# Performance work log

Hardware: AMD Instinct MI355X
Metric: run time of the kernel (lower is better)

Reference implementation:

```python
import jax, jax.numpy as jnp
import numpy as np

N = 50000        # nodes
E = 800000       # edges (avg degree 16)
D_IN = 19        # in_channels(16) + 2 coords + 1 observed flag
H = 64           # graph_hidden
L = 3            # graph_layers
EPS = 1e-5       # BatchNorm eps


def setup_inputs() -> dict:
    key = jax.random.key(0)
    ks = jax.random.split(key, 12)
    s = 0.05
    x = jax.random.normal(ks[0], (N, D_IN), jnp.float32)
    edge_index = jax.random.randint(ks[1], (2, E), 0, N, dtype=jnp.int32)
    return {
        "x": x,
        "edge_index": edge_index,
        # input projection + input BN
        "w_in": jax.random.normal(ks[2], (D_IN, H), jnp.float32) * s,
        "b_in": jnp.zeros((H,), jnp.float32),
        "bn0_g": jnp.ones((H,), jnp.float32),
        "bn0_b": jnp.zeros((H,), jnp.float32),
        # per-layer SAGEConv: lin_l (aggregated neighbors, with bias), lin_r (self, no bias)
        "wl": jax.random.normal(ks[3], (L, H, H), jnp.float32) * s,
        "bl": jnp.zeros((L, H), jnp.float32),
        "wr": jax.random.normal(ks[4], (L, H, H), jnp.float32) * s,
        # per-layer BatchNorm affine
        "bn_g": jnp.ones((L, H), jnp.float32),
        "bn_b": jnp.zeros((L, H), jnp.float32),
    }


def _batchnorm(h, g, b):
    # training-mode BN over the node axis (biased variance, like torch)
    mu = h.mean(axis=0)
    var = h.var(axis=0)
    return (h - mu) * jax.lax.rsqrt(var + EPS) * g + b


def reference(x, edge_index, w_in, b_in, bn0_g, bn0_b, wl, bl, wr, bn_g, bn_b):
    src = edge_index[0]
    dst = edge_index[1]
    n = x.shape[0]

    # input_proj -> BN -> ReLU  (dropout is identity at inference)
    h = x @ w_in + b_in
    h = jax.nn.relu(_batchnorm(h, bn0_g, bn0_b))

    # in-degree for mean aggregation (computed once)
    deg = jax.ops.segment_sum(jnp.ones((src.shape[0],), h.dtype), dst, num_segments=n)
    denom = jnp.maximum(deg, 1.0)[:, None]

    for l in range(L):
        # SAGEConv(mean): gather source feats, segment-mean into targets
        msgs = h[src]                                        # [E, H] gather
        agg = jax.ops.segment_sum(msgs, dst, num_segments=n) / denom
        h_new = agg @ wl[l] + bl[l] + h @ wr[l]
        h_new = jax.nn.relu(_batchnorm(h_new, bn_g[l], bn_b[l]))
        h = h + h_new                                        # residual
    return h
```

## Files before the change

kernel.cpp:

```cpp
#include <hip/hip_runtime.h>
#include <hip/hip_bf16.h>

#define NODES 50000
#define EDGES 800000
#define DIN   19
#define LAYERS 3
#define BN_EPS 1e-5f

#define NBINS 196
#define EPB   4096
#define NBLK  196
#define NTILES 782
#define G0TILES 196
#define APPLY_BLOCKS 2048
#define TPB   256

typedef __attribute__((ext_vector_type(4))) float f32x4;
typedef __attribute__((ext_vector_type(2))) float f32x2;
typedef __attribute__((ext_vector_type(8))) short s16x8;

__device__ inline ushort bf16bits(float f) {
    __hip_bfloat16 h = __float2bfloat16(f);
    return *reinterpret_cast<ushort*>(&h);
}

#if __has_builtin(__builtin_amdgcn_cvt_pk_f32_fp8) && __has_builtin(__builtin_amdgcn_cvt_pk_fp8_f32)
__device__ inline unsigned pack4_fp8(float a, float b, float c, float d) {
    unsigned w = __builtin_amdgcn_cvt_pk_fp8_f32(a, b, 0u, false);
    return __builtin_amdgcn_cvt_pk_fp8_f32(c, d, w, true);
}
__device__ inline void acc4_fp8(unsigned v, float& a0, float& a1, float& a2, float& a3) {
    f32x2 lo = __builtin_amdgcn_cvt_pk_f32_fp8(v, false);
    f32x2 hi = __builtin_amdgcn_cvt_pk_f32_fp8(v, true);
    a0 += lo.x; a1 += lo.y; a2 += hi.x; a3 += hi.y;
}
#else
__device__ inline unsigned enc1(float f) {
    _Float16 hf = (_Float16)f;
    unsigned u = (unsigned)*reinterpret_cast<unsigned short*>(&hf);
    u = (u + 0x7Fu + ((u >> 8) & 1u)) >> 8;
    return u & 0xFFu;
}
__device__ inline float dec1(unsigned b) {
    unsigned short u = (unsigned short)(b << 8);
    _Float16 hf = *reinterpret_cast<_Float16*>(&u);
    return (float)hf;
}
__device__ inline unsigned pack4_fp8(float a, float b, float c, float d) {
    return enc1(a) | (enc1(b) << 8) | (enc1(c) << 16) | (enc1(d) << 24);
}
__device__ inline void acc4_fp8(unsigned v, float& a0, float& a1, float& a2, float& a3) {
    a0 += dec1(v & 0xFF); a1 += dec1((v >> 8) & 0xFF);
    a2 += dec1((v >> 16) & 0xFF); a3 += dec1(v >> 24);
}
#endif


__global__ void k_prep(const float* __restrict__ w_in, const float* __restrict__ wl,
                       const float* __restrict__ wr, ushort* __restrict__ WiT,
                       ushort* __restrict__ WcatT, int* __restrict__ bintot,
                       float* __restrict__ stats) {
    int i0 = blockIdx.x * blockDim.x + threadIdx.x;
    int stride = gridDim.x * blockDim.x;
    for (int i = i0; i < NBINS; i += stride) bintot[i] = 0;
    for (int i = i0; i < 4 * 2048; i += stride) stats[i] = 0.0f;
    for (int i = i0; i < 64 * 32; i += stride) {
        int c = i >> 5, k = i & 31;
        WiT[i] = bf16bits(k < DIN ? w_in[k * 64 + c] : 0.0f);
    }
    for (int i = i0; i < LAYERS * 64 * 128; i += stride) {
        int l = i >> 13, rem = i & 8191;
        int c = rem >> 7, k = rem & 127;
        float v = (k < 64) ? wl[(l * 64 + k) * 64 + c] : wr[(l * 64 + (k - 64)) * 64 + c];
        WcatT[i] = bf16bits(v);
    }
}


union SMemK2 {
    struct { int hist[256], cur[256], wsum[4]; unsigned stage[EPB]; } sort;
    struct { ushort xt[256][40]; float red[4][4][128]; } g0;
};

__device__ inline void do_sortA(int blk, int t, const int* __restrict__ src,
                                const int* __restrict__ dst, int2* __restrict__ cb,
                                int* __restrict__ bintot, unsigned* __restrict__ bbuf,
                                SMemK2& sm) {
    int e0 = blk * EPB;
    int ne = min(EPB, EDGES - e0);
    int d[4]; unsigned pk[4];
    #pragma unroll
    for (int i = 0; i < 4; ++i) {
        int j = t + i * 1024;
        if (j < ne) {
            int dd = dst[e0 + j];
            d[i] = dd;
            pk[i] = ((unsigned)(dd & 255) << 24) | (unsigned)src[e0 + j];
        } else d[i] = -1;
    }
    if (t < 256) sm.sort.hist[t] = 0;
    __syncthreads();
    #pragma unroll
    for (int i = 0; i < 4; ++i)
        if (d[i] >= 0) atomicAdd(&sm.sort.hist[d[i] >> 8], 1);
    __syncthreads();
    int ln = t & 63, wv = t >> 6;
    int cntv = 0, inc = 0;
    if (t < 256) {
        cntv = sm.sort.hist[t];
        inc = cntv;
        #pragma unroll
        for (int s = 1; s < 64; s <<= 1) {
            int u = __shfl_up(inc, s);
            if (ln >= s) inc += u;
        }
        if (ln == 63) sm.sort.wsum[wv] = inc;
    }
    __syncthreads();
    if (t < 256) {
        int woff = 0;
        #pragma unroll
        for (int i = 0; i < 4; ++i) if (i < wv) woff += sm.sort.wsum[i];
        int excl = woff + inc - cntv;
        sm.sort.cur[t] = excl;
        if (t < NBINS) {
            cb[t * NBLK + blk] = make_int2(excl, cntv);
            if (cntv) atomicAdd(&bintot[t], cntv);
        }
    }
    __syncthreads();
    #pragma unroll
    for (int i = 0; i < 4; ++i)
        if (d[i] >= 0) {
            int slot = atomicAdd(&sm.sort.cur[d[i] >> 8], 1);
            sm.sort.stage[slot] = pk[i];
        }
    __syncthreads();
    #pragma unroll
    for (int i = 0; i < 4; ++i) {
        int j = t + i * 1024;
        if (j < ne) bbuf[e0 + j] = sm.sort.stage[j];
    }
}

__device__ inline void do_gemm0(int tile, int t, const float* __restrict__ x,
                                const ushort* __restrict__ WiT, const float* __restrict__ bias,
                                ushort* __restrict__ tb, float* __restrict__ stats,
                                SMemK2& sm) {
    int base = tile * 256;
    int nv = min(256, NODES - base);
    unsigned* xz = (unsigned*)sm.g0.xt;
    for (int i = t; i < 256 * 20; i += 1024) xz[i] = 0;
    __syncthreads();
    const float* xs = x + (size_t)base * DIN;
    for (int e = t; e < nv * DIN; e += 1024) {
        int n = e / DIN, k = e - n * DIN;
        sm.g0.xt[n][k] = bf16bits(xs[e]);
    }
    __syncthreads();
    int grp = t >> 8, tl = t & 255;
    int lane = t & 63, wl = (tl >> 6);
    int r = lane & 15, g = lane >> 4;
    f32x4 acc[4] = {{0.f,0.f,0.f,0.f},{0.f,0.f,0.f,0.f},{0.f,0.f,0.f,0.f},{0.f,0.f,0.f,0.f}};
    s16x8 af = *(const s16x8*)&sm.g0.xt[grp * 64 + wl * 16 + r][g * 8];
    #pragma unroll
    for (int j = 0; j < 4; ++j) {
        s16x8 bf = *(const s16x8*)(WiT + (size_t)(j * 16 + r) * 32 + g * 8);
        acc[j] = __builtin_amdgcn_mfma_f32_16x16x32_bf16(af, bf, acc[j], 0, 0, 0);
    }
    int row0 = base + grp * 64 + wl * 16;
    float s_[4], q_[4];
    #pragma unroll
    for (int j = 0; j < 4; ++j) {
        float b = bias[j * 16 + r];
        float s = 0.0f, q = 0.0f;
        #pragma unroll
        for (int i = 0; i < 4; ++i) {
            int row = row0 + g * 4 + i;
            if (row < NODES) {
                float v = acc[j][i] + b;
                tb[(size_t)row * 64 + j * 16 + r] = bf16bits(v);
                s += v; q += v * v;
            }
        }
        s += __shfl_xor(s, 16); s += __shfl_xor(s, 32);
        q += __shfl_xor(q, 16); q += __shfl_xor(q, 32);
        s_[j] = s; q_[j] = q;
    }
    if (g == 0) {
        #pragma unroll
        for (int j = 0; j < 4; ++j) {
            sm.g0.red[grp][wl][j * 16 + r] = s_[j];
            sm.g0.red[grp][wl][64 + j * 16 + r] = q_[j];
        }
    }
    __syncthreads();
    if (tl < 128) {
        float tot = sm.g0.red[grp][0][tl] + sm.g0.red[grp][1][tl] +
                    sm.g0.red[grp][2][tl] + sm.g0.red[grp][3][tl];
        atomicAdd(&stats[tl * 16], tot);
    }
}

__global__ __launch_bounds__(1024) void k_sort_g0(const int* __restrict__ esrc, const int* __restrict__ edst,
                                                  int2* __restrict__ cb, int* __restrict__ bintot,
                                                  unsigned* __restrict__ bbuf,
                                                  const float* __restrict__ x, const ushort* __restrict__ WiT,
                                                  const float* __restrict__ bias, ushort* __restrict__ tb,
                                                  float* __restrict__ stats) {
    __shared__ SMemK2 sm;
    int t = threadIdx.x;
    if (blockIdx.x < NBLK) do_sortA(blockIdx.x, t, esrc, edst, cb, bintot, bbuf, sm);
    else                   do_gemm0(blockIdx.x - NBLK, t, x, WiT, bias, tb, stats, sm);
}


__device__ inline int ubound(const int* pre, int f) {
    int lo = 0, hi = NBLK;
    while (lo + 1 < hi) {
        int mid = (lo + hi) >> 1;
        if (pre[mid] <= f) lo = mid; else hi = mid;
    }
    return lo;
}

struct SMemBinB {
    int red[256];
    int segoff[NBLK], segcnt[NBLK], pre[NBLK + 1];
    int deg[256], loff[256], cur[256];
    int wsum4[4];
};

__device__ inline void do_binB(int b, int t, const int2* __restrict__ cb,
                               const int* __restrict__ bintot, const unsigned* __restrict__ bbuf,
                               int* __restrict__ off, float* __restrict__ rden,
                               int* __restrict__ ebuf, SMemBinB& sm) {
    int ln = t & 63, wv = t >> 6;
    sm.red[t] = (t < b) ? bintot[t] : 0;
    __syncthreads();
    #pragma unroll
    for (int s = 128; s > 0; s >>= 1) {
        if (t < s) sm.red[t] += sm.red[t + s];
        __syncthreads();
    }
    int binoff = sm.red[0];
    if (t < NBLK) {
        int2 c = cb[b * NBLK + t];
        sm.segoff[t] = c.x; sm.segcnt[t] = c.y;
    }
    sm.deg[t] = 0; sm.cur[t] = 0;
    __syncthreads();
    if (wv == 0) {
        int carry = 0;
        for (int base = 0; base < NBLK; base += 64) {
            int idx = base + ln;
            int v = (idx < NBLK) ? sm.segcnt[idx] : 0;
            int inc = v;
            #pragma unroll
            for (int s = 1; s < 64; s <<= 1) {
                int u = __shfl_up(inc, s);
                if (ln >= s) inc += u;
            }
            if (idx < NBLK) sm.pre[idx] = carry + inc - v;
            carry += __shfl(inc, 63);
        }
        if (ln == 0) sm.pre[NBLK] = carry;
    }
    __syncthreads();
    int total = sm.pre[NBLK];
    for (int f = t; f < total; f += TPB) {
        int sg = ubound(sm.pre, f);
        unsigned e = bbuf[sg * EPB + sm.segoff[sg] + (f - sm.pre[sg])];
        atomicAdd(&sm.deg[e >> 24], 1);
    }
    __syncthreads();
    int dv = sm.deg[t], inc2 = dv;
    #pragma unroll
    for (int s = 1; s < 64; s <<= 1) {
        int u = __shfl_up(inc2, s);
        if (ln >= s) inc2 += u;
    }
    if (ln == 63) sm.wsum4[wv] = inc2;
    __syncthreads();
    int woff = 0;
    #pragma unroll
    for (int i = 0; i < 4; ++i) if (i < wv) woff += sm.wsum4[i];
    int excl = woff + inc2 - dv;
    sm.loff[t] = excl;
    int node = (b << 8) + t;
    if (node < NODES) {
        off[node] = binoff + excl;
        rden[node] = 1.0f / fmaxf((float)dv, 1.0f);
    }
    if (b == NBINS - 1 && t == 0) off[NODES] = EDGES;
    __syncthreads();
    for (int f = t; f < total; f += TPB) {
        int sg = ubound(sm.pre, f);
        unsigned e = bbuf[sg * EPB + sm.segoff[sg] + (f - sm.pre[sg])];
        int dd = e >> 24;
        int slot = atomicAdd(&sm.cur[dd], 1);
        ebuf[binoff + sm.loff[dd] + slot] = (int)(e & 0xFFFFFFu);
    }
}

__device__ inline void do_apply(int idx0, int stride, const ushort* __restrict__ tb,
                                const float* __restrict__ stats, const float* __restrict__ gamma,
                                const float* __restrict__ beta, float* __restrict__ h,
                                ushort* __restrict__ AB, unsigned* __restrict__ hb8,
                                int residual, int write_next) {
    const float invN = 1.0f / NODES;
    for (int idx = idx0; idx < NODES * 16; idx += stride) {
        int n = idx >> 4;
        int j = (idx & 15) * 4;
        ushort4 tv = *(const ushort4*)(tb + (size_t)n * 64 + j);
        float tf[4] = { __uint_as_float((unsigned)tv.x << 16), __uint_as_float((unsigned)tv.y << 16),
                        __uint_as_float((unsigned)tv.z << 16), __uint_as_float((unsigned)tv.w << 16) };
        f32x4 hv;
        if (residual) hv = *(const f32x4*)(h + (size_t)n * 64 + j);
        float out[4];
        ushort ub[4];
        #pragma unroll
        for (int k = 0; k < 4; ++k) {
            int f = j + k;
            float mu = stats[f * 16] * invN;
            float var = stats[(64 + f) * 16] * invN - mu * mu;
            float sc = gamma[f] * rsqrtf(var + BN_EPS);
            float sh = beta[f] - mu * sc;
            float v = fmaxf(tf[k] * sc + sh, 0.0f);
            out[k] = residual ? (hv[k] + v) : v;
            ub[k] = bf16bits(out[k]);
        }
        *(f32x4*)(h + (size_t)n * 64 + j) = f32x4{out[0], out[1], out[2], out[3]};
        if (write_next) {
            *(ushort4*)(AB + (size_t)n * 128 + 64 + j) = make_ushort4(ub[0], ub[1], ub[2], ub[3]);
            hb8[(size_t)n * 16 + (idx & 15)] = pack4_fp8(out[0], out[1], out[2], out[3]);
        }
    }
}

__global__ __launch_bounds__(TPB) void k_csr_bn0(const int2* __restrict__ cb, const int* __restrict__ bintot,
                                                 const unsigned* __restrict__ bbuf,
                                                 int* __restrict__ off, float* __restrict__ rden,
                                                 int* __restrict__ ebuf,
                                                 const ushort* __restrict__ tb, const float* __restrict__ stats,
                                                 const float* __restrict__ gamma, const float* __restrict__ beta,
                                                 float* __restrict__ h, ushort* __restrict__ AB,
                                                 unsigned* __restrict__ hb8) {
    __shared__ SMemBinB sm;
    int t = threadIdx.x;
    if (blockIdx.x < NBINS) {
        do_binB(blockIdx.x, t, cb, bintot, bbuf, off, rden, ebuf, sm);
    } else {
        int vb = blockIdx.x - NBINS;
        do_apply(vb * TPB + t, APPLY_BLOCKS * TPB, tb, stats, gamma, beta, h, AB, hb8, 0, 1);
    }
}


__global__ __launch_bounds__(TPB) void k_gemm(const ushort* __restrict__ AB, const ushort* __restrict__ WT,
                                              const float* __restrict__ bias, ushort* __restrict__ tb,
                                              float* __restrict__ stats) {
    __shared__ float red[4][128];
    int t = threadIdx.x;
    int lane = t & 63, wave = t >> 6;
    int row0 = blockIdx.x * 64;
    int r = lane & 15, g = lane >> 4;
    f32x4 acc[4] = {{0.f,0.f,0.f,0.f},{0.f,0.f,0.f,0.f},{0.f,0.f,0.f,0.f},{0.f,0.f,0.f,0.f}};
    int ar = row0 + wave * 16 + r;
    if (ar >= NODES) ar = NODES - 1;
    #pragma unroll
    for (int k0 = 0; k0 < 128; k0 += 32) {
        s16x8 af = *(const s16x8*)(AB + (size_t)ar * 128 + k0 + g * 8);
        #pragma unroll
        for (int j = 0; j < 4; ++j) {
            s16x8 bf = *(const s16x8*)(WT + (size_t)(j * 16 + r) * 128 + k0 + g * 8);
            acc[j] = __builtin_amdgcn_mfma_f32_16x16x32_bf16(af, bf, acc[j], 0, 0, 0);
        }
    }
    float s_[4], q_[4];
    #pragma unroll
    for (int j = 0; j < 4; ++j) {
        float b = bias[j * 16 + r];
        float s = 0.0f, q = 0.0f;
        #pragma unroll
        for (int i = 0; i < 4; ++i) {
            int row = row0 + wave * 16 + g * 4 + i;
            if (row < NODES) {
                float v = acc[j][i] + b;
                tb[(size_t)row * 64 + j * 16 + r] = bf16bits(v);
                s += v; q += v * v;
            }
        }
        s += __shfl_xor(s, 16); s += __shfl_xor(s, 32);
        q += __shfl_xor(q, 16); q += __shfl_xor(q, 32);
        s_[j] = s; q_[j] = q;
    }
    if (g == 0) {
        #pragma unroll
        for (int j = 0; j < 4; ++j) {
            red[wave][j * 16 + r] = s_[j];
            red[wave][64 + j * 16 + r] = q_[j];
        }
    }
    __syncthreads();
    if (t < 128) {
        float tot = red[0][t] + red[1][t] + red[2][t] + red[3][t];
        atomicAdd(&stats[t * 16], tot);
    }
}


__global__ void k_apply(const ushort* __restrict__ tb, const float* __restrict__ stats,
                        const float* __restrict__ gamma, const float* __restrict__ beta,
                        float* __restrict__ h, ushort* __restrict__ AB,
                        unsigned* __restrict__ hb8, int residual, int write_next) {
    do_apply(blockIdx.x * blockDim.x + threadIdx.x, gridDim.x * blockDim.x,
             tb, stats, gamma, beta, h, AB, hb8, residual, write_next);
}


__global__ void k_agg(const int* __restrict__ off, const int* __restrict__ ebuf,
                      const float* __restrict__ rden, const unsigned* __restrict__ hb8,
                      ushort* __restrict__ ABh) {
    unsigned* AB = (unsigned*)ABh;
    int t = threadIdx.x;
    int lane = t & 63;
    int q = lane >> 4;
    int fl = lane & 15;
    int w = blockIdx.x * (blockDim.x >> 6) + (t >> 6);
    int nw = gridDim.x * (blockDim.x >> 6);
    for (int n = w; n < NODES; n += nw) {
        int p0 = off[n], p1 = off[n + 1];
        float a0 = 0.f, a1 = 0.f, a2 = 0.f, a3 = 0.f;
        int p = p0 + q;
        for (; p + 12 < p1; p += 16) {
            int s0 = ebuf[p], s1 = ebuf[p + 4], s2 = ebuf[p + 8], s3 = ebuf[p + 12];
            unsigned v0 = hb8[(size_t)s0 * 16 + fl];
            unsigned v1 = hb8[(size_t)s1 * 16 + fl];
            unsigned v2 = hb8[(size_t)s2 * 16 + fl];
            unsigned v3 = hb8[(size_t)s3 * 16 + fl];
            acc4_fp8(v0, a0, a1, a2, a3);
            acc4_fp8(v1, a0, a1, a2, a3);
            acc4_fp8(v2, a0, a1, a2, a3);
            acc4_fp8(v3, a0, a1, a2, a3);
        }
        for (; p < p1; p += 4) {
            unsigned v = hb8[(size_t)ebuf[p] * 16 + fl];
            acc4_fp8(v, a0, a1, a2, a3);
        }
        a0 += __shfl_xor(a0, 16); a0 += __shfl_xor(a0, 32);
        a1 += __shfl_xor(a1, 16); a1 += __shfl_xor(a1, 32);
        a2 += __shfl_xor(a2, 16); a2 += __shfl_xor(a2, 32);
        a3 += __shfl_xor(a3, 16); a3 += __shfl_xor(a3, 32);
        if (q == 0) {
            float rd = rden[n];
            uint2 o;
            o.x = (unsigned)bf16bits(a0 * rd) | ((unsigned)bf16bits(a1 * rd) << 16);
            o.y = (unsigned)bf16bits(a2 * rd) | ((unsigned)bf16bits(a3 * rd) << 16);
            *(uint2*)(AB + (size_t)n * 64 + fl * 2) = o;
        }
    }
}


extern "C" void kernel_launch(void* const* d_in, const int* in_sizes, int n_in,
                              void* d_out, int out_size, void* d_ws, size_t ws_size,
                              hipStream_t stream) {
    const float* x    = (const float*)d_in[0];
    const int*   ei   = (const int*)d_in[1];
    const float* w_in = (const float*)d_in[2];
    const float* b_in = (const float*)d_in[3];
    const float* bn0g = (const float*)d_in[4];
    const float* bn0b = (const float*)d_in[5];
    const float* wl   = (const float*)d_in[6];
    const float* bl   = (const float*)d_in[7];
    const float* wr   = (const float*)d_in[8];
    const float* bng  = (const float*)d_in[9];
    const float* bnb  = (const float*)d_in[10];
    const int* esrc = ei;
    const int* edst = ei + EDGES;
    float* h = (float*)d_out;

    char* p = (char*)d_ws;
    auto alloc = [&](size_t bytes) {
        char* r = p;
        p += (bytes + 255) & ~size_t(255);
        return r;
    };
    int*      bintot = (int*)alloc((size_t)NBINS * 4);
    float*    stats  = (float*)alloc((size_t)4 * 2048 * 4);
    int2*     cb     = (int2*)alloc((size_t)NBINS * NBLK * 8);
    unsigned* bbuf   = (unsigned*)alloc((size_t)NBLK * EPB * 4);
    int*      off    = (int*)alloc((size_t)(NODES + 1) * 4);
    float*    rden   = (float*)alloc((size_t)NODES * 4);
    int*      ebuf   = (int*)alloc((size_t)EDGES * 4);
    ushort*   WiT    = (ushort*)alloc(64 * 32 * 2);
    ushort*   WcatT  = (ushort*)alloc(LAYERS * 64 * 128 * 2);
    ushort*   tb     = (ushort*)alloc((size_t)NODES * 64 * 2);
    ushort*   AB     = (ushort*)alloc((size_t)NODES * 128 * 2);
    unsigned* hb8    = (unsigned*)alloc((size_t)NODES * 16 * 4);

    k_prep<<<128, TPB, 0, stream>>>(w_in, wl, wr, WiT, WcatT, bintot, stats);
    k_sort_g0<<<NBLK + G0TILES, 1024, 0, stream>>>(esrc, edst, cb, bintot, bbuf,
                                                   x, WiT, b_in, tb, stats);
    k_csr_bn0<<<NBINS + APPLY_BLOCKS, TPB, 0, stream>>>(cb, bintot, bbuf, off, rden, ebuf,
                                                        tb, stats, bn0g, bn0b, h, AB, hb8);

    for (int l = 0; l < LAYERS; ++l) {
        k_agg<<<2048, TPB, 0, stream>>>(off, ebuf, rden, hb8, AB);
        k_gemm<<<NTILES, TPB, 0, stream>>>(AB, WcatT + l * 8192, bl + l * 64,
                                           tb, stats + (l + 1) * 2048);
        k_apply<<<APPLY_BLOCKS, TPB, 0, stream>>>(tb, stats + (l + 1) * 2048, bng + l * 64,
                                                  bnb + l * 64, h, AB, hb8, 1,
                                                  l < LAYERS - 1 ? 1 : 0);
    }
}
```

Measured before the change: 279.1 us.

## Fuse self-term GEMM into BN apply and widen aggregation gathers

The BN/ReLU/residual apply pass now also computes the next layer's self term (h @ wr + bias) with MFMA on a 64-row tile held in shared memory, storing it as a bf16 buffer. The layer GEMM then only multiplies the 64-wide aggregated features and adds that precomputed term, so the bf16 copy of h in the concatenated AB buffer is no longer written or re-read. The aggregation kernel is restructured so each lane gathers 8 fp8 bytes per edge, with 8 edges in flight per wave. The cost is an extra bf16 intermediate rounding of the self term, plus fewer apply blocks (one per 64-row tile instead of a grid-stride loop).

```diff
diff --git a/kernel.cpp b/kernel.cpp
--- a/kernel.cpp
+++ b/kernel.cpp
@@ -12,7 +12,6 @@
 #define NBLK  196
 #define NTILES 782
 #define G0TILES 196
-#define APPLY_BLOCKS 2048
 #define TPB   256
 
 typedef __attribute__((ext_vector_type(4))) float f32x4;
@@ -23,16 +22,17 @@
     __hip_bfloat16 h = __float2bfloat16(f);
     return *reinterpret_cast<ushort*>(&h);
 }
+__device__ inline float bf16val(ushort u) { return __uint_as_float((unsigned)u << 16); }
 
 #if __has_builtin(__builtin_amdgcn_cvt_pk_f32_fp8) && __has_builtin(__builtin_amdgcn_cvt_pk_fp8_f32)
 __device__ inline unsigned pack4_fp8(float a, float b, float c, float d) {
     unsigned w = __builtin_amdgcn_cvt_pk_fp8_f32(a, b, 0u, false);
     return __builtin_amdgcn_cvt_pk_fp8_f32(c, d, w, true);
 }
-__device__ inline void acc4_fp8(unsigned v, float& a0, float& a1, float& a2, float& a3) {
+__device__ inline void acc4_fp8(unsigned v, float* a) {
     f32x2 lo = __builtin_amdgcn_cvt_pk_f32_fp8(v, false);
     f32x2 hi = __builtin_amdgcn_cvt_pk_f32_fp8(v, true);
-    a0 += lo.x; a1 += lo.y; a2 += hi.x; a3 += hi.y;
+    a[0] += lo.x; a[1] += lo.y; a[2] += hi.x; a[3] += hi.y;
 }
 #else
 __device__ inline unsigned enc1(float f) {
@@ -49,9 +49,9 @@
 __device__ inline unsigned pack4_fp8(float a, float b, float c, float d) {
     return enc1(a) | (enc1(b) << 8) | (enc1(c) << 16) | (enc1(d) << 24);
 }
-__device__ inline void acc4_fp8(unsigned v, float& a0, float& a1, float& a2, float& a3) {
-    a0 += dec1(v & 0xFF); a1 += dec1((v >> 8) & 0xFF);
-    a2 += dec1((v >> 16) & 0xFF); a3 += dec1(v >> 24);
+__device__ inline void acc4_fp8(unsigned v, float* a) {
+    a[0] += dec1(v & 0xFF); a[1] += dec1((v >> 8) & 0xFF);
+    a[2] += dec1((v >> 16) & 0xFF); a[3] += dec1(v >> 24);
 }
 #endif
 
@@ -215,6 +215,75 @@
 }
 
 
+struct SMemApplyR {
+    ushort hn[64][72];
+};
+
+__device__ inline void do_applyR(int rb, int t, int l,
+                                 const ushort* __restrict__ tb, const float* __restrict__ stats,
+                                 const float* __restrict__ gamma, const float* __restrict__ beta,
+                                 float* __restrict__ h, unsigned* __restrict__ hb8,
+                                 const ushort* __restrict__ WcatT, const float* __restrict__ bl,
+                                 ushort* __restrict__ tb2, int residual, SMemApplyR& sm) {
+    const float invN = 1.0f / NODES;
+    int base = rb * 64;
+    int nv = min(64, NODES - base);
+    for (int idx = t; idx < nv * 16; idx += TPB) {
+        int n = base + (idx >> 4);
+        int j = (idx & 15) * 4;
+        ushort4 tv = *(const ushort4*)(tb + (size_t)n * 64 + j);
+        float tf[4] = { bf16val(tv.x), bf16val(tv.y), bf16val(tv.z), bf16val(tv.w) };
+        f32x4 hv;
+        if (residual) hv = *(const f32x4*)(h + (size_t)n * 64 + j);
+        float out[4];
+        #pragma unroll
+        for (int k = 0; k < 4; ++k) {
+            int f = j + k;
+            float mu = stats[f * 16] * invN;
+            float var = stats[(64 + f) * 16] * invN - mu * mu;
+            float sc = gamma[f] * rsqrtf(var + BN_EPS);
+            float sh = beta[f] - mu * sc;
+            float v = fmaxf(tf[k] * sc + sh, 0.0f);
+            out[k] = residual ? (hv[k] + v) : v;
+            sm.hn[idx >> 4][j + k] = bf16bits(out[k]);
+        }
+        *(f32x4*)(h + (size_t)n * 64 + j) = f32x4{out[0], out[1], out[2], out[3]};
+        hb8[(size_t)n * 16 + (idx & 15)] = pack4_fp8(out[0], out[1], out[2], out[3]);
+    }
+    __syncthreads();
+    int lane = t & 63, wave = t >> 6;
+    int r = lane & 15, g = lane >> 4;
+    f32x4 acc[4] = {{0.f,0.f,0.f,0.f},{0.f,0.f,0.f,0.f},{0.f,0.f,0.f,0.f},{0.f,0.f,0.f,0.f}};
+    #pragma unroll
+    for (int k0 = 0; k0 < 64; k0 += 32) {
+        s16x8 af = *(const s16x8*)&sm.hn[wave * 16 + r][k0 + g * 8];
+        #pragma unroll
+        for (int j = 0; j < 4; ++j) {
+            s16x8 bf = *(const s16x8*)(WcatT + (size_t)l * 8192 + (size_t)(j * 16 + r) * 128 + 64 + k0 + g * 8);
+            acc[j] = __builtin_amdgcn_mfma_f32_16x16x32_bf16(af, bf, acc[j], 0, 0, 0);
+        }
+    }
+    #pragma unroll
+    for (int j = 0; j < 4; ++j) {
+        float b = bl[j * 16 + r];
+        #pragma unroll
+        for (int i = 0; i < 4; ++i) {
+            int row = base + wave * 16 + g * 4 + i;
+            if (row < NODES) tb2[(size_t)row * 64 + j * 16 + r] = bf16bits(acc[j][i] + b);
+        }
+    }
+}
+
+__global__ __launch_bounds__(TPB) void k_applyR(const ushort* __restrict__ tb, const float* __restrict__ stats,
+                                                const float* __restrict__ gamma, const float* __restrict__ beta,
+                                                float* __restrict__ h, unsigned* __restrict__ hb8,
+                                                const ushort* __restrict__ WcatT, const float* __restrict__ bl,
+                                                ushort* __restrict__ tb2, int l, int residual) {
+    __shared__ SMemApplyR sm;
+    do_applyR(blockIdx.x, threadIdx.x, l, tb, stats, gamma, beta, h, hb8, WcatT, bl, tb2, residual, sm);
+}
+
+
 __device__ inline int ubound(const int* pre, int f) {
     int lo = 0, hi = NBLK;
     while (lo + 1 < hi) {
@@ -229,6 +298,11 @@
     int segoff[NBLK], segcnt[NBLK], pre[NBLK + 1];
     int deg[256], loff[256], cur[256];
     int wsum4[4];
+};
+
+union SMemK3 {
+    SMemBinB binb;
+    SMemApplyR ar;
 };
 
 __device__ inline void do_binB(int b, int t, const int2* __restrict__ cb,
@@ -303,63 +377,27 @@
     }
 }
 
-__device__ inline void do_apply(int idx0, int stride, const ushort* __restrict__ tb,
-                                const float* __restrict__ stats, const float* __restrict__ gamma,
-                                const float* __restrict__ beta, float* __restrict__ h,
-                                ushort* __restrict__ AB, unsigned* __restrict__ hb8,
-                                int residual, int write_next) {
-    const float invN = 1.0f / NODES;
-    for (int idx = idx0; idx < NODES * 16; idx += stride) {
-        int n = idx >> 4;
-        int j = (idx & 15) * 4;
-        ushort4 tv = *(const ushort4*)(tb + (size_t)n * 64 + j);
-        float tf[4] = { __uint_as_float((unsigned)tv.x << 16), __uint_as_float((unsigned)tv.y << 16),
-                        __uint_as_float((unsigned)tv.z << 16), __uint_as_float((unsigned)tv.w << 16) };
-        f32x4 hv;
-        if (residual) hv = *(const f32x4*)(h + (size_t)n * 64 + j);
-        float out[4];
-        ushort ub[4];
-        #pragma unroll
-        for (int k = 0; k < 4; ++k) {
-            int f = j + k;
-            float mu = stats[f * 16] * invN;
-            float var = stats[(64 + f) * 16] * invN - mu * mu;
-            float sc = gamma[f] * rsqrtf(var + BN_EPS);
-            float sh = beta[f] - mu * sc;
-            float v = fmaxf(tf[k] * sc + sh, 0.0f);
-            out[k] = residual ? (hv[k] + v) : v;
-            ub[k] = bf16bits(out[k]);
-        }
-        *(f32x4*)(h + (size_t)n * 64 + j) = f32x4{out[0], out[1], out[2], out[3]};
-        if (write_next) {
-            *(ushort4*)(AB + (size_t)n * 128 + 64 + j) = make_ushort4(ub[0], ub[1], ub[2], ub[3]);
-            hb8[(size_t)n * 16 + (idx & 15)] = pack4_fp8(out[0], out[1], out[2], out[3]);
-        }
-    }
-}
-
-__global__ __launch_bounds__(TPB) void k_csr_bn0(const int2* __restrict__ cb, const int* __restrict__ bintot,
+__global__ __launch_bounds__(TPB) void k_csr_ar0(const int2* __restrict__ cb, const int* __restrict__ bintot,
                                                  const unsigned* __restrict__ bbuf,
                                                  int* __restrict__ off, float* __restrict__ rden,
                                                  int* __restrict__ ebuf,
                                                  const ushort* __restrict__ tb, const float* __restrict__ stats,
                                                  const float* __restrict__ gamma, const float* __restrict__ beta,
-                                                 float* __restrict__ h, ushort* __restrict__ AB,
-                                                 unsigned* __restrict__ hb8) {
-    __shared__ SMemBinB sm;
+                                                 float* __restrict__ h, unsigned* __restrict__ hb8,
+                                                 const ushort* __restrict__ WcatT, const float* __restrict__ bl,
+                                                 ushort* __restrict__ tb2) {
+    __shared__ SMemK3 sm;
     int t = threadIdx.x;
-    if (blockIdx.x < NBINS) {
-        do_binB(blockIdx.x, t, cb, bintot, bbuf, off, rden, ebuf, sm);
-    } else {
-        int vb = blockIdx.x - NBINS;
-        do_apply(vb * TPB + t, APPLY_BLOCKS * TPB, tb, stats, gamma, beta, h, AB, hb8, 0, 1);
-    }
-}
-
-
-__global__ __launch_bounds__(TPB) void k_gemm(const ushort* __restrict__ AB, const ushort* __restrict__ WT,
-                                              const float* __restrict__ bias, ushort* __restrict__ tb,
-                                              float* __restrict__ stats) {
+    if (blockIdx.x < NBINS)
+        do_binB(blockIdx.x, t, cb, bintot, bbuf, off, rden, ebuf, sm.binb);
+    else
+        do_applyR(blockIdx.x - NBINS, t, 0, tb, stats, gamma, beta, h, hb8, WcatT, bl, tb2, 0, sm.ar);
+}
+
+
+__global__ __launch_bounds__(TPB) void k_gemmL(const ushort* __restrict__ AB, const ushort* __restrict__ WcatT,
+                                               const ushort* __restrict__ tb2, ushort* __restrict__ tb,
+                                               float* __restrict__ stats, int l) {
     __shared__ float red[4][128];
     int t = threadIdx.x;
     int lane = t & 63, wave = t >> 6;
@@ -369,24 +407,23 @@
     int ar = row0 + wave * 16 + r;
     if (ar >= NODES) ar = NODES - 1;
     #pragma unroll
-    for (int k0 = 0; k0 < 128; k0 += 32) {
-        s16x8 af = *(const s16x8*)(AB + (size_t)ar * 128 + k0 + g * 8);
+    for (int k0 = 0; k0 < 64; k0 += 32) {
+        s16x8 af = *(const s16x8*)(AB + (size_t)ar * 64 + k0 + g * 8);
         #pragma unroll
         for (int j = 0; j < 4; ++j) {
-            s16x8 bf = *(const s16x8*)(WT + (size_t)(j * 16 + r) * 128 + k0 + g * 8);
+            s16x8 bf = *(const s16x8*)(WcatT + (size_t)l * 8192 + (size_t)(j * 16 + r) * 128 + k0 + g * 8);
             acc[j] = __builtin_amdgcn_mfma_f32_16x16x32_bf16(af, bf, acc[j], 0, 0, 0);
         }
     }
     float s_[4], q_[4];
     #pragma unroll
     for (int j = 0; j < 4; ++j) {
-        float b = bias[j * 16 + r];
         float s = 0.0f, q = 0.0f;
         #pragma unroll
         for (int i = 0; i < 4; ++i) {
             int row = row0 + wave * 16 + g * 4 + i;
             if (row < NODES) {
-                float v = acc[j][i] + b;
+                float v = acc[j][i] + bf16val(tb2[(size_t)row * 64 + j * 16 + r]);
                 tb[(size_t)row * 64 + j * 16 + r] = bf16bits(v);
                 s += v; q += v * v;
             }
@@ -410,54 +447,73 @@
 }
 
 
-__global__ void k_apply(const ushort* __restrict__ tb, const float* __restrict__ stats,
-                        const float* __restrict__ gamma, const float* __restrict__ beta,
-                        float* __restrict__ h, ushort* __restrict__ AB,
-                        unsigned* __restrict__ hb8, int residual, int write_next) {
-    do_apply(blockIdx.x * blockDim.x + threadIdx.x, gridDim.x * blockDim.x,
-             tb, stats, gamma, beta, h, AB, hb8, residual, write_next);
+__global__ void k_apply_fin(const ushort* __restrict__ tb, const float* __restrict__ stats,
+                            const float* __restrict__ gamma, const float* __restrict__ beta,
+                            float* __restrict__ h) {
+    int idx0 = blockIdx.x * blockDim.x + threadIdx.x;
+    int stride = gridDim.x * blockDim.x;
+    const float invN = 1.0f / NODES;
+    for (int idx = idx0; idx < NODES * 16; idx += stride) {
+        int n = idx >> 4;
+        int j = (idx & 15) * 4;
+        ushort4 tv = *(const ushort4*)(tb + (size_t)n * 64 + j);
+        float tf[4] = { bf16val(tv.x), bf16val(tv.y), bf16val(tv.z), bf16val(tv.w) };
+        f32x4 hv = *(const f32x4*)(h + (size_t)n * 64 + j);
+        float out[4];
+        #pragma unroll
+        for (int k = 0; k < 4; ++k) {
+            int f = j + k;
+            float mu = stats[f * 16] * invN;
+            float var = stats[(64 + f) * 16] * invN - mu * mu;
+            float sc = gamma[f] * rsqrtf(var + BN_EPS);
+            float sh = beta[f] - mu * sc;
+            out[k] = hv[k] + fmaxf(tf[k] * sc + sh, 0.0f);
+        }
+        *(f32x4*)(h + (size_t)n * 64 + j) = f32x4{out[0], out[1], out[2], out[3]};
+    }
 }
 
 
 __global__ void k_agg(const int* __restrict__ off, const int* __restrict__ ebuf,
                       const float* __restrict__ rden, const unsigned* __restrict__ hb8,
                       ushort* __restrict__ ABh) {
-    unsigned* AB = (unsigned*)ABh;
+    const uint2* H2 = (const uint2*)hb8;
+    uint4* AB4 = (uint4*)ABh;
     int t = threadIdx.x;
     int lane = t & 63;
-    int q = lane >> 4;
-    int fl = lane & 15;
+    int q = lane >> 3;
+    int fl = lane & 7;
     int w = blockIdx.x * (blockDim.x >> 6) + (t >> 6);
     int nw = gridDim.x * (blockDim.x >> 6);
     for (int n = w; n < NODES; n += nw) {
         int p0 = off[n], p1 = off[n + 1];
-        float a0 = 0.f, a1 = 0.f, a2 = 0.f, a3 = 0.f;
+        float a[8] = {0.f,0.f,0.f,0.f,0.f,0.f,0.f,0.f};
         int p = p0 + q;
-        for (; p + 12 < p1; p += 16) {
-            int s0 = ebuf[p], s1 = ebuf[p + 4], s2 = ebuf[p + 8], s3 = ebuf[p + 12];
-            unsigned v0 = hb8[(size_t)s0 * 16 + fl];
-            unsigned v1 = hb8[(size_t)s1 * 16 + fl];
-            unsigned v2 = hb8[(size_t)s2 * 16 + fl];
-            unsigned v3 = hb8[(size_t)s3 * 16 + fl];
-            acc4_fp8(v0, a0, a1, a2, a3);
-            acc4_fp8(v1, a0, a1, a2, a3);
-            acc4_fp8(v2, a0, a1, a2, a3);
-            acc4_fp8(v3, a0, a1, a2, a3);
-        }
-        for (; p < p1; p += 4) {
-            unsigned v = hb8[(size_t)ebuf[p] * 16 + fl];
-            acc4_fp8(v, a0, a1, a2, a3);
-        }
-        a0 += __shfl_xor(a0, 16); a0 += __shfl_xor(a0, 32);
-        a1 += __shfl_xor(a1, 16); a1 += __shfl_xor(a1, 32);
-        a2 += __shfl_xor(a2, 16); a2 += __shfl_xor(a2, 32);
-        a3 += __shfl_xor(a3, 16); a3 += __shfl_xor(a3, 32);
+        for (; p + 8 < p1; p += 16) {
+            int s0 = ebuf[p], s1 = ebuf[p + 8];
+            uint2 v0 = H2[(size_t)s0 * 8 + fl];
+            uint2 v1 = H2[(size_t)s1 * 8 + fl];
+            acc4_fp8(v0.x, a); acc4_fp8(v0.y, a + 4);
+            acc4_fp8(v1.x, a); acc4_fp8(v1.y, a + 4);
+        }
+        for (; p < p1; p += 8) {
+            uint2 v = H2[(size_t)ebuf[p] * 8 + fl];
+            acc4_fp8(v.x, a); acc4_fp8(v.y, a + 4);
+        }
+        #pragma unroll
+        for (int i = 0; i < 8; ++i) {
+            a[i] += __shfl_xor(a[i], 8);
+            a[i] += __shfl_xor(a[i], 16);
+            a[i] += __shfl_xor(a[i], 32);
+        }
         if (q == 0) {
             float rd = rden[n];
-            uint2 o;
-            o.x = (unsigned)bf16bits(a0 * rd) | ((unsigned)bf16bits(a1 * rd) << 16);
-            o.y = (unsigned)bf16bits(a2 * rd) | ((unsigned)bf16bits(a3 * rd) << 16);
-            *(uint2*)(AB + (size_t)n * 64 + fl * 2) = o;
+            uint4 o;
+            o.x = (unsigned)bf16bits(a[0] * rd) | ((unsigned)bf16bits(a[1] * rd) << 16);
+            o.y = (unsigned)bf16bits(a[2] * rd) | ((unsigned)bf16bits(a[3] * rd) << 16);
+            o.z = (unsigned)bf16bits(a[4] * rd) | ((unsigned)bf16bits(a[5] * rd) << 16);
+            o.w = (unsigned)bf16bits(a[6] * rd) | ((unsigned)bf16bits(a[7] * rd) << 16);
+            AB4[(size_t)n * 8 + fl] = o;
         }
     }
 }
@@ -497,21 +553,27 @@
     ushort*   WiT    = (ushort*)alloc(64 * 32 * 2);
     ushort*   WcatT  = (ushort*)alloc(LAYERS * 64 * 128 * 2);
     ushort*   tb     = (ushort*)alloc((size_t)NODES * 64 * 2);
-    ushort*   AB     = (ushort*)alloc((size_t)NODES * 128 * 2);
+    ushort*   tb2    = (ushort*)alloc((size_t)NODES * 64 * 2);
+    ushort*   AB     = (ushort*)alloc((size_t)NODES * 64 * 2);
     unsigned* hb8    = (unsigned*)alloc((size_t)NODES * 16 * 4);
 
     k_prep<<<128, TPB, 0, stream>>>(w_in, wl, wr, WiT, WcatT, bintot, stats);
     k_sort_g0<<<NBLK + G0TILES, 1024, 0, stream>>>(esrc, edst, cb, bintot, bbuf,
                                                    x, WiT, b_in, tb, stats);
-    k_csr_bn0<<<NBINS + APPLY_BLOCKS, TPB, 0, stream>>>(cb, bintot, bbuf, off, rden, ebuf,
-                                                        tb, stats, bn0g, bn0b, h, AB, hb8);
+    k_csr_ar0<<<NBINS + NTILES, TPB, 0, stream>>>(cb, bintot, bbuf, off, rden, ebuf,
+                                                  tb, stats, bn0g, bn0b, h, hb8,
+                                                  WcatT, bl + 0 * 64, tb2);
 
     for (int l = 0; l < LAYERS; ++l) {
         k_agg<<<2048, TPB, 0, stream>>>(off, ebuf, rden, hb8, AB);
-        k_gemm<<<NTILES, TPB, 0, stream>>>(AB, WcatT + l * 8192, bl + l * 64,
-                                           tb, stats + (l + 1) * 2048);
-        k_apply<<<APPLY_BLOCKS, TPB, 0, stream>>>(tb, stats + (l + 1) * 2048, bng + l * 64,
-                                                  bnb + l * 64, h, AB, hb8, 1,
-                                                  l < LAYERS - 1 ? 1 : 0);
-    }
-}
+        k_gemmL<<<NTILES, TPB, 0, stream>>>(AB, WcatT, tb2, tb, stats + (l + 1) * 2048, l);
+        if (l < LAYERS - 1) {
+            k_applyR<<<NTILES, TPB, 0, stream>>>(tb, stats + (l + 1) * 2048, bng + l * 64,
+                                                 bnb + l * 64, h, hb8, WcatT,
+                                                 bl + (l + 1) * 64, tb2, l + 1, 1);
+        } else {
+            k_apply_fin<<<2048, TPB, 0, stream>>>(tb, stats + (l + 1) * 2048, bng + l * 64,
+                                                  bnb + l * 64, h);
+        }
+    }
+}
```

New measurement: 261.3 us, median of 2. -6.4%, faster.
